# Performance work log

Hardware: AMD Instinct MI355X
Metric: run time of the kernel (lower is better)

Reference implementation:

```python
import jax, jax.numpy as jnp
import numpy as np

DIM = 768
HEADS = 12
DIM_HEAD = 64
INNER = HEADS * DIM_HEAD  # 768
EPS = 1e-5


def setup_inputs() -> dict:
    key = jax.random.key(0)
    ks = jax.random.split(key, 5)
    x = jax.random.normal(ks[0], (4, 2048, DIM), dtype=jnp.float32)
    ln_g = jnp.ones((DIM,), dtype=jnp.float32)
    ln_b = jnp.zeros((DIM,), dtype=jnp.float32)
    s1 = 1.0 / np.sqrt(DIM)
    W_qkv = jax.random.uniform(ks[1], (DIM, 3 * INNER), dtype=jnp.float32, minval=-s1, maxval=s1)
    b_qkv = jax.random.uniform(ks[2], (3 * INNER,), dtype=jnp.float32, minval=-s1, maxval=s1)
    s2 = 1.0 / np.sqrt(INNER)
    W_out = jax.random.uniform(ks[3], (INNER, DIM), dtype=jnp.float32, minval=-s2, maxval=s2)
    b_out = jax.random.uniform(ks[4], (DIM,), dtype=jnp.float32, minval=-s2, maxval=s2)
    return {"x": x, "ln_g": ln_g, "ln_b": ln_b, "W_qkv": W_qkv, "b_qkv": b_qkv, "W_out": W_out, "b_out": b_out}


def reference(x, ln_g, ln_b, W_qkv, b_qkv, W_out, b_out):
    b, n, _ = x.shape
    # pre-norm LayerNorm
    mu = jnp.mean(x, axis=-1, keepdims=True)
    var = jnp.mean(jnp.square(x - mu), axis=-1, keepdims=True)
    xn = (x - mu) * jax.lax.rsqrt(var + EPS) * ln_g + ln_b
    qkv = xn @ W_qkv + b_qkv  # [b, n, 3*inner]
    q, k, v = jnp.split(qkv, 3, axis=-1)
    def to_heads(t):
        return t.reshape(b, n, HEADS, DIM_HEAD).transpose(0, 2, 1, 3)  # b h n d
    q, k, v = map(to_heads, (q, k, v))
    q = q * (DIM_HEAD ** -0.5)
    sim = jnp.einsum('bhid,bhjd->bhij', q, k)
    attn = jax.nn.softmax(sim, axis=-1)  # dropout is identity (p=0.0)
    out = jnp.einsum('bhij,bhjd->bhid', attn, v)
    out = out.transpose(0, 2, 1, 3).reshape(b, n, INNER)
    return out @ W_out + b_out
```

## Files before the change

kernel.cpp:

```cpp
#include <hip/hip_runtime.h>
#include <cstdint>
#include <cstddef>


#define SEQ    2048
#define NBATCH 4
#define DMODEL 768
#define NHEADS 12
#define DHEAD  64
#define MROWS  (NBATCH * SEQ)
#define NQKV   (3 * DMODEL)
#define KT     64
#define NT     (SEQ / KT)

using f32x4  = __attribute__((ext_vector_type(4))) float;
using u16x8  = __attribute__((ext_vector_type(8))) unsigned short;
using s16x8  = __attribute__((ext_vector_type(8))) short;
using u16x4  = __attribute__((ext_vector_type(4))) unsigned short;
using s16x4  = __attribute__((ext_vector_type(4))) short;

__device__ __forceinline__ unsigned short f2bf(float f) {
  union { float f; unsigned int u; } x; x.f = f;
  unsigned int r = x.u + 0x7fffu + ((x.u >> 16) & 1u);
  return (unsigned short)(r >> 16);
}

#if defined(__has_builtin)
#if __has_builtin(__builtin_amdgcn_cvt_pk_bf16_f32)
#define HAVE_PK_BF16 1
#endif
#if __has_builtin(__builtin_amdgcn_exp2f)
#define HAVE_EXP2 1
#endif
#if __has_builtin(__builtin_amdgcn_mfma_f32_16x16x16bf16_1k)
#define HAVE_MFMA_16X16X16_BF16 1
#endif
#endif

__device__ __forceinline__ unsigned int pk_bf16(float a, float b) {
#ifdef HAVE_PK_BF16
  auto v = __builtin_amdgcn_cvt_pk_bf16_f32(a, b);
  union { decltype(v) v2; unsigned int u; } c; c.v2 = v; return c.u;
#else
  return (unsigned int)f2bf(a) | ((unsigned int)f2bf(b) << 16);
#endif
}

__device__ __forceinline__ float fexp2(float x) {
#ifdef HAVE_EXP2
  return __builtin_amdgcn_exp2f(x);
#else
  return exp2f(x);
#endif
}

__device__ __forceinline__ f32x4 mfma16(u16x8 a, u16x8 b, f32x4 c) {
  return __builtin_amdgcn_mfma_f32_16x16x32_bf16((s16x8)a, (s16x8)b, c, 0, 0, 0);
}

__device__ __forceinline__ f32x4 mfma16k16(u16x4 a, u16x4 b, f32x4 c) {
#ifdef HAVE_MFMA_16X16X16_BF16
  return __builtin_amdgcn_mfma_f32_16x16x16bf16_1k((s16x4)a, (s16x4)b, c, 0, 0, 0);
#else
  f32x4 d;
  asm("v_mfma_f32_16x16x16_bf16 %0, %1, %2, %3"
      : "=v"(d) : "v"(a), "v"(b), "v"(c));
  return d;
#endif
}

__device__ __forceinline__ void gl_lds16(const void* g, void* l) {
  __builtin_amdgcn_global_load_lds(
      (const __attribute__((address_space(1))) void*)g,
      (__attribute__((address_space(3))) void*)l, 16, 0, 0);
}

__global__ __launch_bounds__(256) void ln_kernel(
    const float* __restrict__ x, const float* __restrict__ g,
    const float* __restrict__ bb, unsigned short* __restrict__ xn) {
  __shared__ float red[8];
  const int row = blockIdx.x, t = threadIdx.x;
  const float* xr = x + (size_t)row * DMODEL;
  float v0 = xr[t], v1 = xr[t + 256], v2 = xr[t + 512];
  float s = v0 + v1 + v2;
#pragma unroll
  for (int o = 32; o; o >>= 1) s += __shfl_down(s, o);
  if ((t & 63) == 0) red[t >> 6] = s;
  __syncthreads();
  float mu = (red[0] + red[1] + red[2] + red[3]) * (1.0f / DMODEL);
  float d0 = v0 - mu, d1 = v1 - mu, d2 = v2 - mu;
  float q = d0 * d0 + d1 * d1 + d2 * d2;
#pragma unroll
  for (int o = 32; o; o >>= 1) q += __shfl_down(q, o);
  if ((t & 63) == 0) red[4 + (t >> 6)] = q;
  __syncthreads();
  float var = (red[4] + red[5] + red[6] + red[7]) * (1.0f / DMODEL);
  float rstd = rsqrtf(var + 1e-5f);
  size_t base = (size_t)row * DMODEL;
  xn[base + t]       = f2bf(d0 * rstd * g[t]       + bb[t]);
  xn[base + t + 256] = f2bf(d1 * rstd * g[t + 256] + bb[t + 256]);
  xn[base + t + 512] = f2bf(d2 * rstd * g[t + 512] + bb[t + 512]);
}

__global__ __launch_bounds__(256) void tconv_kernel(
    const float* __restrict__ W, unsigned short* __restrict__ Wt, int N) {
  __shared__ float tile[32][33];
  const int n0 = blockIdx.x * 32, k0 = blockIdx.y * 32;
  const int tx = threadIdx.x & 31, ty = threadIdx.x >> 5;
#pragma unroll
  for (int r = 0; r < 4; ++r)
    tile[ty + r * 8][tx] = W[(size_t)(k0 + ty + r * 8) * N + n0 + tx];
  __syncthreads();
#pragma unroll
  for (int r = 0; r < 4; ++r)
    Wt[(size_t)(n0 + ty + r * 8) * DMODEL + k0 + tx] = f2bf(tile[tx][ty + r * 8]);
}

__global__ __launch_bounds__(256, 2) void gemm_qkv_kernel(
    const unsigned short* __restrict__ Wt, const unsigned short* __restrict__ xn,
    const float* __restrict__ bias, unsigned short* __restrict__ qb,
    unsigned short* __restrict__ kb, unsigned short* __restrict__ vt) {
  __shared__ alignas(16) unsigned short As[128 * 64];
  __shared__ alignas(16) unsigned short Bs[128 * 64];
  const int t = threadIdx.x, wid = t >> 6, l = t & 63, quad = l >> 4, ll = l & 15;
  const int bid = blockIdx.x;
  const int w = (bid & 7) * 144 + (bid >> 3);
  const bool isqk = (w < 768);
  int a0, b0;
  if (isqk) { a0 = (w % 12) * 128; b0 = (w / 12) * 128; }
  else { int w2 = w - 768; a0 = (w2 & 63) * 128; b0 = 2 * DMODEL + (w2 >> 6) * 128; }
  const unsigned short* Ap = isqk ? (Wt + (size_t)a0 * DMODEL) : (xn + (size_t)a0 * DMODEL);
  const unsigned short* Bp = isqk ? (xn + (size_t)b0 * DMODEL) : (Wt + (size_t)b0 * DMODEL);
  const int wa = (wid >> 1) * 64, wb = (wid & 1) * 64;
  const int srow = l >> 3, sblk = (l & 7) ^ srow;
  f32x4 acc[4][4] = {};
  for (int k0 = 0; k0 < DMODEL; k0 += 64) {
#pragma unroll
    for (int cc = 0; cc < 4; ++cc) {
      int call = wid * 4 + cc;
      int r = call * 8 + srow;
      gl_lds16(Ap + (size_t)r * DMODEL + k0 + sblk * 8, &As[call * 512]);
      gl_lds16(Bp + (size_t)r * DMODEL + k0 + sblk * 8, &Bs[call * 512]);
    }
    __syncthreads();
#pragma unroll
    for (int ks = 0; ks < 2; ++ks) {
      u16x8 af[4], bf[4];
#pragma unroll
      for (int i = 0; i < 4; ++i) {
        int ra = wa + i * 16 + ll, rb = wb + i * 16 + ll;
        int blk = (ks * 4 + quad) ^ (ll & 7);
        af[i] = *(const u16x8*)&As[ra * 64 + blk * 8];
        bf[i] = *(const u16x8*)&Bs[rb * 64 + blk * 8];
      }
#pragma unroll
      for (int mi = 0; mi < 4; ++mi)
#pragma unroll
        for (int ni = 0; ni < 4; ++ni)
          acc[mi][ni] = mfma16(af[mi], bf[ni], acc[mi][ni]);
    }
    __syncthreads();
  }
  if (isqk) {
    const bool isq = (a0 < DMODEL);
    unsigned short* dst = isq ? qb : kb;
    const float sc = isq ? 0.18033688f : 1.0f;
#pragma unroll
    for (int mi = 0; mi < 4; ++mi) {
      int row0 = a0 + wa + mi * 16 + quad * 4;
      float4 bv = *(const float4*)&bias[row0];
      int rr = isq ? row0 : row0 - DMODEL;
      int h = rr >> 6, d0 = rr & 63;
#pragma unroll
      for (int ni = 0; ni < 4; ++ni) {
        int seq = b0 + wb + ni * 16 + ll;
        int b = seq >> 11, i = seq & 2047;
        uint2 pk;
        pk.x = pk_bf16((acc[mi][ni][0] + bv.x) * sc, (acc[mi][ni][1] + bv.y) * sc);
        pk.y = pk_bf16((acc[mi][ni][2] + bv.z) * sc, (acc[mi][ni][3] + bv.w) * sc);
        *(uint2*)&dst[(size_t)((b * NHEADS + h) * SEQ + i) * DHEAD + d0] = pk;
      }
    }
  } else {
#pragma unroll
    for (int mi = 0; mi < 4; ++mi) {
      int gm = a0 + wa + mi * 16 + quad * 4;
      int b = gm >> 11, i0 = gm & 2047;
#pragma unroll
      for (int ni = 0; ni < 4; ++ni) {
        int gn = b0 + wb + ni * 16 + ll;
        float bv = bias[gn];
        int rem = gn - 2 * DMODEL;
        int h = rem >> 6, d = rem & 63;
        int bh = b * NHEADS + h;
        uint2 pk;
        pk.x = pk_bf16(acc[mi][ni][0] + bv, acc[mi][ni][1] + bv);
        pk.y = pk_bf16(acc[mi][ni][2] + bv, acc[mi][ni][3] + bv);
        *(uint2*)&vt[((size_t)bh * DHEAD + d) * SEQ + i0] = pk;
      }
    }
  }
}

__global__ __launch_bounds__(512, 4) void attn_kernel(
    const unsigned short* __restrict__ qbuf, const unsigned short* __restrict__ kbuf,
    const unsigned short* __restrict__ vtg, unsigned short* __restrict__ ao) {
  __shared__ alignas(16) unsigned short stage[2][2][KT * DHEAD];
  const int t = threadIdx.x, wid = t >> 6, l = t & 63, quad = l >> 4, ll = l & 15;
  const int qg = wid >> 1, kg = wid & 1;
  const int Lid = blockIdx.y * 16 + blockIdx.x;
  const int w = (Lid & 7) * 96 + (Lid >> 3);
  const int qt = w & 15, bh = w >> 4;
  const unsigned short* qg_ = qbuf + ((size_t)bh * SEQ + qt * 128) * DHEAD;
  const unsigned short* kg0 = kbuf + (size_t)bh * SEQ * DHEAD;
  const unsigned short* vt0 = vtg  + (size_t)bh * DHEAD * SEQ;
  const int srow = l >> 3;
  const int sblk = (l & 7) ^ srow;

  unsigned short* Qs = &stage[0][0][0];
#pragma unroll
  for (int cc = 0; cc < 2; ++cc) {
    int call = wid * 2 + cc;
    gl_lds16(qg_ + (call * 8 + srow) * 64 + sblk * 8, Qs + call * 512);
  }
  __syncthreads();
  u16x8 qf[2][2];
#pragma unroll
  for (int mi = 0; mi < 2; ++mi)
#pragma unroll
    for (int ks = 0; ks < 2; ++ks) {
      int r = qg * 32 + mi * 16 + ll;
      int blk = (ks * 4 + quad) ^ (ll & 7);
      qf[mi][ks] = *(const u16x8*)&Qs[r * 64 + blk * 8];
    }
  __syncthreads();

  auto stage_tile = [&](int buf, int kt2) {
    const unsigned short* kg_p = kg0 + (size_t)kt2 * KT * DHEAD;
    int r = wid * 8 + srow;
    gl_lds16(kg_p + r * 64 + sblk * 8, &stage[buf][0][wid * 512]);
    gl_lds16(vt0 + (size_t)r * SEQ + kt2 * KT + sblk * 8, &stage[buf][1][wid * 512]);
  };

  f32x4 oacc[2][4] = {};
  f32x4 osum[2] = {};
  const u16x4 onesb = {0x3f80u, 0x3f80u, 0x3f80u, 0x3f80u};

  stage_tile(0, 0);
  int buf = 0;
  for (int kt2 = 0; kt2 < NT; ++kt2) {
    __syncthreads();
    if (kt2 + 1 < NT) stage_tile(buf ^ 1, kt2 + 1);
    const unsigned short* Ks = &stage[buf][0][0];
    const unsigned short* Vs = &stage[buf][1][0];

    f32x4 st[2][2] = {};
#pragma unroll
    for (int ks = 0; ks < 2; ++ks)
#pragma unroll
      for (int ni = 0; ni < 2; ++ni) {
        int r = kg * 32 + ni * 16 + ll;
        int blk = (ks * 4 + quad) ^ (ll & 7);
        u16x8 kf = *(const u16x8*)&Ks[r * 64 + blk * 8];
        st[0][ni] = mfma16(kf, qf[0][ks], st[0][ni]);
        st[1][ni] = mfma16(kf, qf[1][ks], st[1][ni]);
      }

#pragma unroll
    for (int ni = 0; ni < 2; ++ni) {
      const int nb = kg * 2 + ni;
      u16x4 pf[2];
#pragma unroll
      for (int mi = 0; mi < 2; ++mi) {
        float p0 = fexp2(st[mi][ni][0]);
        float p1 = fexp2(st[mi][ni][1]);
        float p2 = fexp2(st[mi][ni][2]);
        float p3 = fexp2(st[mi][ni][3]);
        union { uint2 u; u16x4 v; } cv;
        cv.u.x = pk_bf16(p0, p1);
        cv.u.y = pk_bf16(p2, p3);
        pf[mi] = cv.v;
        osum[mi] = mfma16k16(pf[mi], onesb, osum[mi]);
      }
      const int voff = (((nb * 2 + (quad >> 1)) ^ (ll & 7)) << 3) + (quad & 1) * 4;
#pragma unroll
      for (int di = 0; di < 4; ++di) {
        u16x4 vf = *(const u16x4*)&Vs[(di * 16 + ll) * 64 + voff];
        oacc[0][di] = mfma16k16(pf[0], vf, oacc[0][di]);
        oacc[1][di] = mfma16k16(pf[1], vf, oacc[1][di]);
      }
    }
    buf ^= 1;
  }

  f32x4* scr = (f32x4*)&stage[0][0][0];
#pragma unroll
  for (int mi = 0; mi < 2; ++mi) {
    __syncthreads();
    f32x4* p = scr + (qg * 64 + l) * 5;
    if (kg) {
      p[0] = oacc[mi][0]; p[1] = oacc[mi][1];
      p[2] = oacc[mi][2]; p[3] = oacc[mi][3]; p[4] = osum[mi];
    }
    __syncthreads();
    if (!kg) {
      oacc[mi][0] += p[0]; oacc[mi][1] += p[1];
      oacc[mi][2] += p[2]; oacc[mi][3] += p[3]; osum[mi] += p[4];
    }
  }

  if (kg == 0) {
    const int b = bh / NHEADS, h = bh - b * NHEADS;
#pragma unroll
    for (int mi = 0; mi < 2; ++mi) {
#pragma unroll
      for (int r = 0; r < 4; ++r) {
        float inv = 1.0f / osum[mi][r];
        int row = qt * 128 + qg * 32 + mi * 16 + quad * 4 + r;
        size_t base = ((size_t)(b * SEQ + row)) * DMODEL + h * DHEAD;
#pragma unroll
        for (int di = 0; di < 4; ++di)
          ao[base + di * 16 + ll] = f2bf(oacc[mi][di][r] * inv);
      }
    }
  }
}

__global__ __launch_bounds__(256, 3) void gemm_out_kernel(
    const unsigned short* __restrict__ Wt, const unsigned short* __restrict__ ao,
    const float* __restrict__ bias, float* __restrict__ out) {
  __shared__ alignas(16) unsigned short As[64 * 64];
  __shared__ alignas(16) unsigned short Bs[128 * 64];
  const int t = threadIdx.x, wid = t >> 6, l = t & 63, quad = l >> 4, ll = l & 15;
  const int a0 = blockIdx.x * 64;
  const int b0 = blockIdx.y * 128;
  const int wa = (wid >> 1) * 32, wb = (wid & 1) * 64;
  const int srow = l >> 3, sblk = (l & 7) ^ srow;
  f32x4 acc[2][4] = {};
  for (int k0 = 0; k0 < DMODEL; k0 += 64) {
#pragma unroll
    for (int cc = 0; cc < 6; ++cc) {
      int call = wid * 6 + cc;
      if (call < 8) {
        int r = call * 8 + srow;
        gl_lds16(Wt + (size_t)(a0 + r) * DMODEL + k0 + sblk * 8, &As[call * 512]);
      } else {
        int c2 = call - 8;
        int r = c2 * 8 + srow;
        gl_lds16(ao + (size_t)(b0 + r) * DMODEL + k0 + sblk * 8, &Bs[c2 * 512]);
      }
    }
    __syncthreads();
#pragma unroll
    for (int ks = 0; ks < 2; ++ks) {
      u16x8 af[2], bf[4];
#pragma unroll
      for (int i = 0; i < 2; ++i) {
        int ra = wa + i * 16 + ll;
        int blk = (ks * 4 + quad) ^ (ll & 7);
        af[i] = *(const u16x8*)&As[ra * 64 + blk * 8];
      }
#pragma unroll
      for (int i = 0; i < 4; ++i) {
        int rb = wb + i * 16 + ll;
        int blk = (ks * 4 + quad) ^ (ll & 7);
        bf[i] = *(const u16x8*)&Bs[rb * 64 + blk * 8];
      }
#pragma unroll
      for (int mi = 0; mi < 2; ++mi)
#pragma unroll
        for (int ni = 0; ni < 4; ++ni)
          acc[mi][ni] = mfma16(af[mi], bf[ni], acc[mi][ni]);
    }
    __syncthreads();
  }
#pragma unroll
  for (int mi = 0; mi < 2; ++mi) {
    int row0 = a0 + wa + mi * 16 + quad * 4;
    float4 bv = *(const float4*)&bias[row0];
#pragma unroll
    for (int ni = 0; ni < 4; ++ni) {
      int seq = b0 + wb + ni * 16 + ll;
      float4 o;
      o.x = acc[mi][ni][0] + bv.x;
      o.y = acc[mi][ni][1] + bv.y;
      o.z = acc[mi][ni][2] + bv.z;
      o.w = acc[mi][ni][3] + bv.w;
      *(float4*)&out[(size_t)seq * DMODEL + row0] = o;
    }
  }
}

extern "C" void kernel_launch(void* const* d_in, const int* in_sizes, int n_in,
                              void* d_out, int out_size, void* d_ws, size_t ws_size,
                              hipStream_t stream) {
  const float* x     = (const float*)d_in[0];
  const float* ln_g  = (const float*)d_in[1];
  const float* ln_b  = (const float*)d_in[2];
  const float* W_qkv = (const float*)d_in[3];
  const float* b_qkv = (const float*)d_in[4];
  const float* W_out = (const float*)d_in[5];
  const float* b_out = (const float*)d_in[6];
  float* out = (float*)d_out;

  char* ws = (char*)d_ws;
  unsigned short* xn    = (unsigned short*)(ws);
  unsigned short* wqkvt = (unsigned short*)(ws + 12582912);
  unsigned short* woutt = (unsigned short*)(ws + 16121856);
  unsigned short* qb    = (unsigned short*)(ws + 17301504);
  unsigned short* kb    = (unsigned short*)(ws + 29884416);
  unsigned short* vt    = (unsigned short*)(ws + 42467328);
  unsigned short* ao    = xn;

  ln_kernel<<<MROWS, 256, 0, stream>>>(x, ln_g, ln_b, xn);
  tconv_kernel<<<dim3(NQKV / 32, DMODEL / 32), 256, 0, stream>>>(W_qkv, wqkvt, NQKV);
  tconv_kernel<<<dim3(DMODEL / 32, DMODEL / 32), 256, 0, stream>>>(W_out, woutt, DMODEL);
  gemm_qkv_kernel<<<1152, 256, 0, stream>>>(wqkvt, xn, b_qkv, qb, kb, vt);
  attn_kernel<<<dim3(SEQ / 128, NBATCH * NHEADS), 512, 0, stream>>>(qb, kb, vt, ao);
  gemm_out_kernel<<<dim3(12, 64), 256, 0, stream>>>(woutt, ao, b_out, out);
}
```

Before: 239.4 us.

## Restructure attention to 4 waves with triple-buffered K/V prefetch and fuse weight transposes

The attention kernel moves from 8 waves that split the key dimension and then reduce across waves to 4 waves, each of which processes the full 64-key tile. The split-K shared-memory reduction goes away. K/V staging becomes a 3-deep ring with two tiles in flight, gated by explicit vmcnt waits and a raw barrier, and MFMA sections are wrapped in s_setprio. The two weight-transpose launches are merged into one kernel, and the QKV GEMM launch bound rises to 3 blocks per CU. The trade-off is more registers per wave, a larger LDS footprint, and less parallelism per block.

```diff
diff --git a/kernel.cpp b/kernel.cpp
--- a/kernel.cpp
+++ b/kernel.cpp
@@ -102,10 +102,14 @@
   xn[base + t + 512] = f2bf(d2 * rstd * g[t + 512] + bb[t + 512]);
 }
 
-__global__ __launch_bounds__(256) void tconv_kernel(
-    const float* __restrict__ W, unsigned short* __restrict__ Wt, int N) {
+__global__ __launch_bounds__(256) void tconv2_kernel(
+    const float* __restrict__ Wq, const float* __restrict__ Wo,
+    unsigned short* __restrict__ Wqt, unsigned short* __restrict__ Wot) {
   __shared__ float tile[32][33];
-  const int n0 = blockIdx.x * 32, k0 = blockIdx.y * 32;
+  int id = blockIdx.x;
+  const float* W; unsigned short* Wt; int N, n0, k0;
+  if (id < 1728) { W = Wq; Wt = Wqt; N = NQKV;   n0 = (id % 72) * 32; k0 = (id / 72) * 32; }
+  else { id -= 1728; W = Wo; Wt = Wot; N = DMODEL; n0 = (id % 24) * 32; k0 = (id / 24) * 32; }
   const int tx = threadIdx.x & 31, ty = threadIdx.x >> 5;
 #pragma unroll
   for (int r = 0; r < 4; ++r)
@@ -116,7 +120,7 @@
     Wt[(size_t)(n0 + ty + r * 8) * DMODEL + k0 + tx] = f2bf(tile[tx][ty + r * 8]);
 }
 
-__global__ __launch_bounds__(256, 2) void gemm_qkv_kernel(
+__global__ __launch_bounds__(256, 3) void gemm_qkv_kernel(
     const unsigned short* __restrict__ Wt, const unsigned short* __restrict__ xn,
     const float* __restrict__ bias, unsigned short* __restrict__ qb,
     unsigned short* __restrict__ kb, unsigned short* __restrict__ vt) {
@@ -202,16 +206,15 @@
   }
 }
 
-__global__ __launch_bounds__(512, 4) void attn_kernel(
+__global__ __launch_bounds__(256, 3) void attn_kernel(
     const unsigned short* __restrict__ qbuf, const unsigned short* __restrict__ kbuf,
     const unsigned short* __restrict__ vtg, unsigned short* __restrict__ ao) {
-  __shared__ alignas(16) unsigned short stage[2][2][KT * DHEAD];
+  __shared__ alignas(16) unsigned short stage[3][2][KT * DHEAD];
   const int t = threadIdx.x, wid = t >> 6, l = t & 63, quad = l >> 4, ll = l & 15;
-  const int qg = wid >> 1, kg = wid & 1;
   const int Lid = blockIdx.y * 16 + blockIdx.x;
   const int w = (Lid & 7) * 96 + (Lid >> 3);
   const int qt = w & 15, bh = w >> 4;
-  const unsigned short* qg_ = qbuf + ((size_t)bh * SEQ + qt * 128) * DHEAD;
+  const unsigned short* qg  = qbuf + ((size_t)bh * SEQ + qt * 128) * DHEAD;
   const unsigned short* kg0 = kbuf + (size_t)bh * SEQ * DHEAD;
   const unsigned short* vt0 = vtg  + (size_t)bh * DHEAD * SEQ;
   const int srow = l >> 3;
@@ -219,9 +222,9 @@
 
   unsigned short* Qs = &stage[0][0][0];
 #pragma unroll
-  for (int cc = 0; cc < 2; ++cc) {
-    int call = wid * 2 + cc;
-    gl_lds16(qg_ + (call * 8 + srow) * 64 + sblk * 8, Qs + call * 512);
+  for (int cc = 0; cc < 4; ++cc) {
+    int call = wid * 4 + cc;
+    gl_lds16(qg + (call * 8 + srow) * 64 + sblk * 8, Qs + call * 512);
   }
   __syncthreads();
   u16x8 qf[2][2];
@@ -229,17 +232,21 @@
   for (int mi = 0; mi < 2; ++mi)
 #pragma unroll
     for (int ks = 0; ks < 2; ++ks) {
-      int r = qg * 32 + mi * 16 + ll;
+      int r = wid * 32 + mi * 16 + ll;
       int blk = (ks * 4 + quad) ^ (ll & 7);
       qf[mi][ks] = *(const u16x8*)&Qs[r * 64 + blk * 8];
     }
   __syncthreads();
 
   auto stage_tile = [&](int buf, int kt2) {
-    const unsigned short* kg_p = kg0 + (size_t)kt2 * KT * DHEAD;
-    int r = wid * 8 + srow;
-    gl_lds16(kg_p + r * 64 + sblk * 8, &stage[buf][0][wid * 512]);
-    gl_lds16(vt0 + (size_t)r * SEQ + kt2 * KT + sblk * 8, &stage[buf][1][wid * 512]);
+    const unsigned short* kg = kg0 + (size_t)kt2 * KT * DHEAD;
+#pragma unroll
+    for (int c = 0; c < 2; ++c) {
+      int call = wid * 2 + c;
+      int r = call * 8 + srow;
+      gl_lds16(kg + r * 64 + sblk * 8, &stage[buf][0][call * 512]);
+      gl_lds16(vt0 + (size_t)r * SEQ + kt2 * KT + sblk * 8, &stage[buf][1][call * 512]);
+    }
   };
 
   f32x4 oacc[2][4] = {};
@@ -247,28 +254,32 @@
   const u16x4 onesb = {0x3f80u, 0x3f80u, 0x3f80u, 0x3f80u};
 
   stage_tile(0, 0);
-  int buf = 0;
+  stage_tile(1, 1);
+  int bufc = 0, bufs = 2;
   for (int kt2 = 0; kt2 < NT; ++kt2) {
-    __syncthreads();
-    if (kt2 + 1 < NT) stage_tile(buf ^ 1, kt2 + 1);
-    const unsigned short* Ks = &stage[buf][0][0];
-    const unsigned short* Vs = &stage[buf][1][0];
-
-    f32x4 st[2][2] = {};
+    if (kt2 + 1 < NT) asm volatile("s_waitcnt vmcnt(4)" ::: "memory");
+    else              asm volatile("s_waitcnt vmcnt(0)" ::: "memory");
+    __builtin_amdgcn_s_barrier();
+    if (kt2 + 2 < NT) stage_tile(bufs, kt2 + 2);
+    const unsigned short* Ks = &stage[bufc][0][0];
+    const unsigned short* Vs = &stage[bufc][1][0];
+
+    f32x4 st[2][4] = {};
+    __builtin_amdgcn_s_setprio(1);
 #pragma unroll
     for (int ks = 0; ks < 2; ++ks)
 #pragma unroll
-      for (int ni = 0; ni < 2; ++ni) {
-        int r = kg * 32 + ni * 16 + ll;
+      for (int ni = 0; ni < 4; ++ni) {
+        int r = ni * 16 + ll;
         int blk = (ks * 4 + quad) ^ (ll & 7);
         u16x8 kf = *(const u16x8*)&Ks[r * 64 + blk * 8];
         st[0][ni] = mfma16(kf, qf[0][ks], st[0][ni]);
         st[1][ni] = mfma16(kf, qf[1][ks], st[1][ni]);
       }
-
-#pragma unroll
-    for (int ni = 0; ni < 2; ++ni) {
-      const int nb = kg * 2 + ni;
+    __builtin_amdgcn_s_setprio(0);
+
+#pragma unroll
+    for (int ni = 0; ni < 4; ++ni) {
       u16x4 pf[2];
 #pragma unroll
       for (int mi = 0; mi < 2; ++mi) {
@@ -280,48 +291,34 @@
         cv.u.x = pk_bf16(p0, p1);
         cv.u.y = pk_bf16(p2, p3);
         pf[mi] = cv.v;
-        osum[mi] = mfma16k16(pf[mi], onesb, osum[mi]);
-      }
-      const int voff = (((nb * 2 + (quad >> 1)) ^ (ll & 7)) << 3) + (quad & 1) * 4;
+      }
+      const int voff = (((ni * 2 + (quad >> 1)) ^ (ll & 7)) << 3) + (quad & 1) * 4;
+      __builtin_amdgcn_s_setprio(1);
+      osum[0] = mfma16k16(pf[0], onesb, osum[0]);
+      osum[1] = mfma16k16(pf[1], onesb, osum[1]);
 #pragma unroll
       for (int di = 0; di < 4; ++di) {
         u16x4 vf = *(const u16x4*)&Vs[(di * 16 + ll) * 64 + voff];
         oacc[0][di] = mfma16k16(pf[0], vf, oacc[0][di]);
         oacc[1][di] = mfma16k16(pf[1], vf, oacc[1][di]);
       }
-    }
-    buf ^= 1;
-  }
-
-  f32x4* scr = (f32x4*)&stage[0][0][0];
+      __builtin_amdgcn_s_setprio(0);
+    }
+    bufc = (bufc == 2) ? 0 : bufc + 1;
+    bufs = (bufs == 2) ? 0 : bufs + 1;
+  }
+
+  const int b = bh / NHEADS, h = bh - b * NHEADS;
 #pragma unroll
   for (int mi = 0; mi < 2; ++mi) {
-    __syncthreads();
-    f32x4* p = scr + (qg * 64 + l) * 5;
-    if (kg) {
-      p[0] = oacc[mi][0]; p[1] = oacc[mi][1];
-      p[2] = oacc[mi][2]; p[3] = oacc[mi][3]; p[4] = osum[mi];
-    }
-    __syncthreads();
-    if (!kg) {
-      oacc[mi][0] += p[0]; oacc[mi][1] += p[1];
-      oacc[mi][2] += p[2]; oacc[mi][3] += p[3]; osum[mi] += p[4];
-    }
-  }
-
-  if (kg == 0) {
-    const int b = bh / NHEADS, h = bh - b * NHEADS;
-#pragma unroll
-    for (int mi = 0; mi < 2; ++mi) {
-#pragma unroll
-      for (int r = 0; r < 4; ++r) {
-        float inv = 1.0f / osum[mi][r];
-        int row = qt * 128 + qg * 32 + mi * 16 + quad * 4 + r;
-        size_t base = ((size_t)(b * SEQ + row)) * DMODEL + h * DHEAD;
-#pragma unroll
-        for (int di = 0; di < 4; ++di)
-          ao[base + di * 16 + ll] = f2bf(oacc[mi][di][r] * inv);
-      }
+#pragma unroll
+    for (int r = 0; r < 4; ++r) {
+      float inv = 1.0f / osum[mi][r];
+      int row = qt * 128 + wid * 32 + mi * 16 + quad * 4 + r;
+      size_t base = ((size_t)(b * SEQ + row)) * DMODEL + h * DHEAD;
+#pragma unroll
+      for (int di = 0; di < 4; ++di)
+        ao[base + di * 16 + ll] = f2bf(oacc[mi][di][r] * inv);
     }
   }
 }
@@ -413,9 +410,8 @@
   unsigned short* ao    = xn;
 
   ln_kernel<<<MROWS, 256, 0, stream>>>(x, ln_g, ln_b, xn);
-  tconv_kernel<<<dim3(NQKV / 32, DMODEL / 32), 256, 0, stream>>>(W_qkv, wqkvt, NQKV);
-  tconv_kernel<<<dim3(DMODEL / 32, DMODEL / 32), 256, 0, stream>>>(W_out, woutt, DMODEL);
+  tconv2_kernel<<<2304, 256, 0, stream>>>(W_qkv, W_out, wqkvt, woutt);
   gemm_qkv_kernel<<<1152, 256, 0, stream>>>(wqkvt, xn, b_qkv, qb, kb, vt);
-  attn_kernel<<<dim3(SEQ / 128, NBATCH * NHEADS), 512, 0, stream>>>(qb, kb, vt, ao);
+  attn_kernel<<<dim3(SEQ / 128, NBATCH * NHEADS), 256, 0, stream>>>(qb, kb, vt, ao);
   gemm_out_kernel<<<dim3(12, 64), 256, 0, stream>>>(woutt, ao, b_out, out);
 }
```

Measured after the change: 226.1 us. 5.5% less time.
